# Kernel tuning notes

Hardware: AMD Instinct MI355X
Metric: run time of the kernel (lower is better)

Reference implementation:

```python
import jax, jax.numpy as jnp
import numpy as np

B = 4096
IN_FEATS = 1024
OUT_FEATS = 1024
NUM_HEADS = 16
NUM_MEMS = 4096
HEAD_DIM = OUT_FEATS // NUM_HEADS
TEMPERATURE = 1.0
EPS = 0.0  # original code uses plain jnp.linalg.norm (no eps)


def setup_inputs() -> dict:
    key = jax.random.key(0)
    k1, k2, k3 = jax.random.split(key, 3)
    x = jax.random.normal(k1, (B, IN_FEATS), dtype=jnp.float32)
    # eqx.nn.Linear stores weight as [out, in]; uniform-like init replaced with normal scaled
    W_q = jax.random.normal(k2, (OUT_FEATS, IN_FEATS), dtype=jnp.float32) * (1.0 / np.sqrt(IN_FEATS))
    memories = jax.random.normal(k3, (NUM_HEADS, NUM_MEMS, HEAD_DIM), dtype=jnp.float32) * 0.02
    return {"x": x, "W_q": W_q, "memories": memories}


def reference(x, W_q, memories):
    # q = query_proj(x): [B, out_feats] -> [B, H, d]
    q = (x @ W_q.T).reshape(B, NUM_HEADS, HEAD_DIM)
    # L2-normalize queries and memories along feature dim
    q_norm = q / jnp.linalg.norm(q, axis=-1, keepdims=True)
    mem_norm = memories / jnp.linalg.norm(memories, axis=-1, keepdims=True)
    # cosine-similarity scores: [B, H, M]
    attn_scores = jnp.einsum('bhd,hmd->bhm', q_norm, mem_norm)
    # soft readout (hard=False branch)
    mem_probs = jax.nn.softmax(attn_scores / TEMPERATURE, axis=-1)
    # weighted combine of normalized memories, scaled by sqrt(head_dim)
    out = jnp.einsum('bhm,hmd->bhd', mem_probs, mem_norm) * jnp.sqrt(HEAD_DIM).astype(x.dtype)
    return out.reshape(B, OUT_FEATS)
```

## Files before the change

kernel.cpp:

```cpp
#include <hip/hip_runtime.h>
#include <stdint.h>

#define B_SZ  4096
#define HEADS 16
#define HD    64
#define M_SZ  4096
#define K_IN  1024
#define SW    72
#define LOG2E 1.44269504088896f

typedef _Float16 f16;
typedef f16  f16x2 __attribute__((ext_vector_type(2)));
typedef f16  f16x4 __attribute__((ext_vector_type(4)));
typedef f16  f16x8 __attribute__((ext_vector_type(8)));
typedef float f32x4 __attribute__((ext_vector_type(4)));

union U8 { uint4 u4; f16x8 h8; unsigned short us[8]; };
union U4 { uint2 u2; f16x4 h4; unsigned int ui[2]; unsigned short us[4]; };

__device__ __forceinline__ unsigned short f2h(float f) {
    _Float16 h = (_Float16)f;
    return __builtin_bit_cast(unsigned short, h);
}
__device__ __forceinline__ f16x8 ldsv8(const unsigned short* p) {
    U8 u; u.u4 = *reinterpret_cast<const uint4*>(p); return u.h8;
}

#if __has_builtin(__builtin_amdgcn_exp2f)
#define EXP2F(x) __builtin_amdgcn_exp2f(x)
#else
#define EXP2F(x) __expf((x) * 0.6931471805599453f)
#endif

__device__ __forceinline__ f16x4 pack4(float a, float b, float c, float d) {
#if __has_builtin(__builtin_amdgcn_cvt_pkrtz)
    U4 u;
    u.ui[0] = __builtin_bit_cast(unsigned int, __builtin_amdgcn_cvt_pkrtz(a, b));
    u.ui[1] = __builtin_bit_cast(unsigned int, __builtin_amdgcn_cvt_pkrtz(c, d));
    return u.h4;
#else
    f16x4 r; r[0] = (f16)a; r[1] = (f16)b; r[2] = (f16)c; r[3] = (f16)d;
    return r;
#endif
}

__global__ __launch_bounds__(256) void k_conv(const float* __restrict__ x,
                                              const float* __restrict__ Wq,
                                              unsigned short* __restrict__ xh,
                                              unsigned short* __restrict__ Wh) {
    const int b = blockIdx.x;
    const float* src;
    unsigned short* dst;
    size_t base;
    if (b < 2048) { src = x;  dst = xh; base = (size_t)b * 2048; }
    else          { src = Wq; dst = Wh; base = (size_t)(b - 2048) * 2048; }
    const size_t i = base + (size_t)threadIdx.x * 8;
    float4 f0 = reinterpret_cast<const float4*>(src + i)[0];
    float4 f1 = reinterpret_cast<const float4*>(src + i)[1];
    U8 u;
    u.us[0] = f2h(f0.x); u.us[1] = f2h(f0.y); u.us[2] = f2h(f0.z); u.us[3] = f2h(f0.w);
    u.us[4] = f2h(f1.x); u.us[5] = f2h(f1.y); u.us[6] = f2h(f1.z); u.us[7] = f2h(f1.w);
    *reinterpret_cast<uint4*>(dst + i) = u.u4;
}

__global__ __launch_bounds__(256) void k_prep_mem(const float* __restrict__ mem,
                                                  unsigned short* __restrict__ Af,
                                                  unsigned short* __restrict__ Bf) {
    __shared__ float part[64][4];
    __shared__ float scale[64];
    __shared__ unsigned short Tn[64 * SW];

    const int h  = blockIdx.y;
    const int tl = blockIdx.x;
    const int m0 = tl * 64;
    const int tid = threadIdx.x;
    const int r = tid >> 2;
    const int c = tid & 3;

    const float* src = mem + ((size_t)(h * M_SZ + m0 + r)) * HD + c * 16;
    float v[16];
    float ss = 0.f;
#pragma unroll
    for (int i = 0; i < 4; i++) {
        float4 f = reinterpret_cast<const float4*>(src)[i];
        v[4*i+0] = f.x; v[4*i+1] = f.y; v[4*i+2] = f.z; v[4*i+3] = f.w;
        ss += f.x*f.x + f.y*f.y + f.z*f.z + f.w*f.w;
    }
    part[r][c] = ss;
    __syncthreads();
    if (tid < 64) {
        float s = part[tid][0] + part[tid][1] + part[tid][2] + part[tid][3];
        scale[tid] = rsqrtf(s);
    }
    __syncthreads();
    const float sc = scale[r];

    U8 a, b;
#pragma unroll
    for (int i = 0; i < 8; i++) { a.us[i] = f2h(v[i] * sc); b.us[i] = f2h(v[8 + i] * sc); }
    *reinterpret_cast<uint4*>(&Tn[r * SW + c * 16])     = a.u4;
    *reinterpret_cast<uint4*>(&Tn[r * SW + c * 16 + 8]) = b.u4;
    __syncthreads();

    const int w = tid >> 6, lane = tid & 63;
    const int l15 = lane & 15, quad = lane >> 4;

#pragma unroll
    for (int i = 0; i < 2; i++) {
        const int gs = w * 2 + i, g = gs >> 1, s = gs & 1;
        uint4 vv = *reinterpret_cast<const uint4*>(&Tn[(g * 16 + l15) * SW + s * 32 + quad * 8]);
        unsigned short* dst = Af + (((size_t)(h * 64 + tl) * 8 + gs) * 64 + lane) * 8;
        *reinterpret_cast<uint4*>(dst) = vv;
    }
#pragma unroll
    for (int i = 0; i < 2; i++) {
        const int gnp = w * 2 + i, g = gnp >> 1, np = gnp & 1;
        U8 u;
#pragma unroll
        for (int j = 0; j < 4; j++) {
            u.us[j]     = Tn[(g * 16 + quad * 4 + j) * SW + (2 * np) * 16 + l15];
            u.us[4 + j] = Tn[(g * 16 + quad * 4 + j) * SW + (2 * np + 1) * 16 + l15];
        }
        unsigned short* dst = Bf + (((size_t)(h * 64 + tl) * 8 + gnp) * 64 + lane) * 8;
        *reinterpret_cast<uint4*>(dst) = u.u4;
    }
}

__global__ __launch_bounds__(256) void k_qproj(const unsigned short* __restrict__ xh,
                                               const unsigned short* __restrict__ Wh,
                                               unsigned short* __restrict__ qn) {
    __shared__ unsigned short sbuf[2 * 128 * SW];
    unsigned short* As = sbuf;
    unsigned short* Bs = sbuf + 128 * SW;

    const int b0 = blockIdx.x * 128;
    const int n0 = blockIdx.y * 128;
    const int t = threadIdx.x;
    const int w = t >> 6, lane = t & 63;
    const int wr = w >> 1, wc = w & 1;
    const int l15 = lane & 15, quad = lane >> 4;

    f32x4 acc[4][4] = {};

    const int sr = t >> 1, sh = (t & 1) * 32;
    for (int kb = 0; kb < K_IN; kb += 64) {
        __syncthreads();
        {
            const unsigned short* px = xh + (size_t)(b0 + sr) * K_IN + kb + sh;
            const unsigned short* pw = Wh + (size_t)(n0 + sr) * K_IN + kb + sh;
            uint4 av[4], bv[4];
#pragma unroll
            for (int i = 0; i < 4; i++) av[i] = reinterpret_cast<const uint4*>(px)[i];
#pragma unroll
            for (int i = 0; i < 4; i++) bv[i] = reinterpret_cast<const uint4*>(pw)[i];
#pragma unroll
            for (int i = 0; i < 4; i++) {
                *reinterpret_cast<uint4*>(&As[sr * SW + sh + i * 8]) = av[i];
                *reinterpret_cast<uint4*>(&Bs[sr * SW + sh + i * 8]) = bv[i];
            }
        }
        __syncthreads();

#pragma unroll
        for (int s = 0; s < 2; s++) {
            f16x8 af[4];
#pragma unroll
            for (int qg = 0; qg < 4; qg++)
                af[qg] = ldsv8(&As[(wr * 64 + qg * 16 + l15) * SW + s * 32 + quad * 8]);
#pragma unroll
            for (int g = 0; g < 4; g++) {
                f16x8 bf_ = ldsv8(&Bs[(wc * 64 + g * 16 + l15) * SW + s * 32 + quad * 8]);
#pragma unroll
                for (int qg = 0; qg < 4; qg++)
                    acc[qg][g] = __builtin_amdgcn_mfma_f32_16x16x32_f16(af[qg], bf_, acc[qg][g], 0, 0, 0);
            }
        }
    }

    __syncthreads();
    unsigned short* Ct = sbuf;
#pragma unroll
    for (int qg = 0; qg < 4; qg++) {
        float ssq[4];
#pragma unroll
        for (int r = 0; r < 4; r++) {
            float s = 0.f;
#pragma unroll
            for (int g = 0; g < 4; g++) s += acc[qg][g][r] * acc[qg][g][r];
            ssq[r] = s;
        }
#pragma unroll
        for (int mask = 1; mask <= 8; mask <<= 1)
#pragma unroll
            for (int r = 0; r < 4; r++) ssq[r] += __shfl_xor(ssq[r], mask, 64);
#pragma unroll
        for (int r = 0; r < 4; r++) {
            float inv = rsqrtf(ssq[r]) * LOG2E;
#pragma unroll
            for (int g = 0; g < 4; g++)
                Ct[(wr * 64 + qg * 16 + quad * 4 + r) * 136 + wc * 64 + g * 16 + l15] =
                    f2h(acc[qg][g][r] * inv);
        }
    }
    __syncthreads();

    const int row = t >> 1, half = (t & 1) * 64;
    unsigned short* dq = qn + (size_t)(b0 + row) * 1024 + n0 + half;
#pragma unroll
    for (int i = 0; i < 8; i++)
        reinterpret_cast<uint4*>(dq)[i] = *reinterpret_cast<const uint4*>(&Ct[row * 136 + half + i * 8]);
}

__global__ __launch_bounds__(256, 2) void k_attn(const unsigned short* __restrict__ qn,
                                                 const unsigned short* __restrict__ Af,
                                                 const unsigned short* __restrict__ Bf,
                                                 float* __restrict__ out) {
    const int b = blockIdx.x;
    const int h  = 2 * (b & 7) + (b >> 8);
    const int b0 = ((b >> 3) & 31) * 128;
    const int t = threadIdx.x;
    const int w = t >> 6, lane = t & 63;
    const int l15 = lane & 15, quad = lane >> 4;

    f16x8 qf[2][2];
#pragma unroll
    for (int qg = 0; qg < 2; qg++)
#pragma unroll
        for (int s = 0; s < 2; s++) {
            U8 u;
            u.u4 = *reinterpret_cast<const uint4*>(
                qn + (size_t)(b0 + w * 32 + qg * 16 + l15) * 1024 + h * 64 + s * 32 + quad * 8);
            qf[qg][s] = u.h8;
        }

    const unsigned short* pA = Af + (size_t)h * 64 * 4096 + lane * 8;
    const unsigned short* pB = Bf + (size_t)h * 64 * 4096 + lane * 8;

    f32x4 accO[2][4] = {};
    float lsum[2] = {0.f, 0.f};

    for (int tl = 0; tl < 64; ++tl) {
        const unsigned short* pAt = pA + (size_t)tl * 4096;
        const unsigned short* pBt = pB + (size_t)tl * 4096;

        f16x8 am[8], bw[8];
#pragma unroll
        for (int gs = 0; gs < 8; gs++) {
            U8 u; u.u4 = *reinterpret_cast<const uint4*>(pAt + gs * 512);
            am[gs] = u.h8;
        }
#pragma unroll
        for (int gnp = 0; gnp < 8; gnp++) {
            U8 u; u.u4 = *reinterpret_cast<const uint4*>(pBt + gnp * 512);
            bw[gnp] = u.h8;
        }

        f16x4 pa[2][4];
#pragma unroll
        for (int qg = 0; qg < 2; qg++) {
#pragma unroll
            for (int g = 0; g < 4; g++) {
                f32x4 sc = {0.f, 0.f, 0.f, 0.f};
                sc = __builtin_amdgcn_mfma_f32_16x16x32_f16(am[g * 2 + 0], qf[qg][0], sc, 0, 0, 0);
                sc = __builtin_amdgcn_mfma_f32_16x16x32_f16(am[g * 2 + 1], qf[qg][1], sc, 0, 0, 0);
                float p0 = EXP2F(sc[0]), p1 = EXP2F(sc[1]);
                float p2 = EXP2F(sc[2]), p3 = EXP2F(sc[3]);
                lsum[qg] += (p0 + p1) + (p2 + p3);
                pa[qg][g] = pack4(p0, p1, p2, p3);
            }
        }

#pragma unroll
        for (int g = 0; g < 4; g++) {
#pragma unroll
            for (int np = 0; np < 2; np++) {
                f16x4 blo = __builtin_shufflevector(bw[g * 2 + np], bw[g * 2 + np], 0, 1, 2, 3);
                f16x4 bhi = __builtin_shufflevector(bw[g * 2 + np], bw[g * 2 + np], 4, 5, 6, 7);
#pragma unroll
                for (int qg = 0; qg < 2; qg++) {
                    accO[qg][2 * np]     = __builtin_amdgcn_mfma_f32_16x16x16f16(pa[qg][g], blo, accO[qg][2 * np], 0, 0, 0);
                    accO[qg][2 * np + 1] = __builtin_amdgcn_mfma_f32_16x16x16f16(pa[qg][g], bhi, accO[qg][2 * np + 1], 0, 0, 0);
                }
            }
        }
    }

#pragma unroll
    for (int qg = 0; qg < 2; qg++) {
        float s = lsum[qg];
        s += __shfl_xor(s, 16, 64);
        s += __shfl_xor(s, 32, 64);
        float inv = 8.0f / s;
#pragma unroll
        for (int r = 0; r < 4; r++) {
            float iv = __shfl(inv, quad * 4 + r, 64);
            float* po = out + (size_t)(b0 + w * 32 + qg * 16 + quad * 4 + r) * 1024 + h * 64;
#pragma unroll
            for (int n = 0; n < 4; n++)
                po[n * 16 + l15] = accO[qg][n][r] * iv;
        }
    }
}

extern "C" void kernel_launch(void* const* d_in, const int* in_sizes, int n_in,
                              void* d_out, int out_size, void* d_ws, size_t ws_size,
                              hipStream_t stream) {
    (void)in_sizes; (void)n_in; (void)out_size; (void)ws_size;
    const float* x   = (const float*)d_in[0];
    const float* Wq  = (const float*)d_in[1];
    const float* mem = (const float*)d_in[2];
    float* out = (float*)d_out;

    unsigned short* qn = (unsigned short*)d_ws;
    unsigned short* Af = qn + (size_t)B_SZ * 1024;
    unsigned short* Bf = Af + (size_t)HEADS * 64 * 4096;
    unsigned short* xh = Bf + (size_t)HEADS * 64 * 4096;
    unsigned short* Wh = xh + (size_t)B_SZ * K_IN;

    k_conv    <<<2560, 256, 0, stream>>>(x, Wq, xh, Wh);
    k_prep_mem<<<dim3(64, 16), 256, 0, stream>>>(mem, Af, Bf);
    k_qproj   <<<dim3(32, 8), 256, 0, stream>>>(xh, Wh, qn);
    k_attn    <<<512, 256, 0, stream>>>(qn, Af, Bf, out);
}
```

Measured before the change: 199.0 us.

## Stage memory tiles via async LDS double-buffering and use 16x16x32 MFMA for PV

The attention kernel now loads each memory tile from global straight into a double-buffered LDS array with global_load_lds, prefetching the next tile while the current one is computed. Previously every wave loaded the same tile from global memory on its own. The memory-prep kernel packs both score and value fragments into one interleaved layout whose row order is permuted, so the probability fragments from the score MFMA feed the 16x16x32 MFMA directly. This halves the MFMA count for the PV product. The q-projection tile shrinks to 128x64 with a grid of 512 blocks for better occupancy. The cost is an extra __syncthreads per tile and 32KB of LDS per block, and the correctness of the permuted row mapping rests on careful index arithmetic.

New measurement: 179.1 us. 1.11x faster.

```diff
diff --git a/kernel.cpp b/kernel.cpp
--- a/kernel.cpp
+++ b/kernel.cpp
@@ -10,13 +10,11 @@
 #define LOG2E 1.44269504088896f
 
 typedef _Float16 f16;
-typedef f16  f16x2 __attribute__((ext_vector_type(2)));
 typedef f16  f16x4 __attribute__((ext_vector_type(4)));
 typedef f16  f16x8 __attribute__((ext_vector_type(8)));
 typedef float f32x4 __attribute__((ext_vector_type(4)));
 
-union U8 { uint4 u4; f16x8 h8; unsigned short us[8]; };
-union U4 { uint2 u2; f16x4 h4; unsigned int ui[2]; unsigned short us[4]; };
+union U8 { uint4 u4; f16x8 h8; unsigned int ui[4]; unsigned short us[8]; };
 
 __device__ __forceinline__ unsigned short f2h(float f) {
     _Float16 h = (_Float16)f;
@@ -32,16 +30,10 @@
 #define EXP2F(x) __expf((x) * 0.6931471805599453f)
 #endif
 
-__device__ __forceinline__ f16x4 pack4(float a, float b, float c, float d) {
-#if __has_builtin(__builtin_amdgcn_cvt_pkrtz)
-    U4 u;
-    u.ui[0] = __builtin_bit_cast(unsigned int, __builtin_amdgcn_cvt_pkrtz(a, b));
-    u.ui[1] = __builtin_bit_cast(unsigned int, __builtin_amdgcn_cvt_pkrtz(c, d));
-    return u.h4;
-#else
-    f16x4 r; r[0] = (f16)a; r[1] = (f16)b; r[2] = (f16)c; r[3] = (f16)d;
-    return r;
-#endif
+__device__ __forceinline__ void gload_lds16(const void* g, void* l) {
+    __builtin_amdgcn_global_load_lds(
+        (const __attribute__((address_space(1))) void*)g,
+        (__attribute__((address_space(3))) void*)l, 16, 0, 0);
 }
 
 __global__ __launch_bounds__(256) void k_conv(const float* __restrict__ x,
@@ -64,8 +56,7 @@
 }
 
 __global__ __launch_bounds__(256) void k_prep_mem(const float* __restrict__ mem,
-                                                  unsigned short* __restrict__ Af,
-                                                  unsigned short* __restrict__ Bf) {
+                                                  unsigned short* __restrict__ F) {
     __shared__ float part[64][4];
     __shared__ float scale[64];
     __shared__ unsigned short Tn[64 * SW];
@@ -104,83 +95,80 @@
 
     const int w = tid >> 6, lane = tid & 63;
     const int l15 = lane & 15, quad = lane >> 4;
+    unsigned short* Fd = F + ((size_t)(h * 64 + tl) * 16) * 512;
 
 #pragma unroll
     for (int i = 0; i < 2; i++) {
-        const int gs = w * 2 + i, g = gs >> 1, s = gs & 1;
-        uint4 vv = *reinterpret_cast<const uint4*>(&Tn[(g * 16 + l15) * SW + s * 32 + quad * 8]);
-        unsigned short* dst = Af + (((size_t)(h * 64 + tl) * 8 + gs) * 64 + lane) * 8;
-        *reinterpret_cast<uint4*>(dst) = vv;
+        const int ch = w * 2 + i, g = ch >> 1, s = ch & 1;
+        const int mp = 32 * (g >> 1) + ((l15 >> 2) * 8) + 4 * (g & 1) + (l15 & 3);
+        uint4 vv = *reinterpret_cast<const uint4*>(&Tn[mp * SW + s * 32 + quad * 8]);
+        *reinterpret_cast<uint4*>(Fd + ch * 512 + lane * 8) = vv;
     }
 #pragma unroll
     for (int i = 0; i < 2; i++) {
-        const int gnp = w * 2 + i, g = gnp >> 1, np = gnp & 1;
+        const int c2 = w * 2 + i, p = c2 >> 2, n = c2 & 3;
         U8 u;
 #pragma unroll
-        for (int j = 0; j < 4; j++) {
-            u.us[j]     = Tn[(g * 16 + quad * 4 + j) * SW + (2 * np) * 16 + l15];
-            u.us[4 + j] = Tn[(g * 16 + quad * 4 + j) * SW + (2 * np + 1) * 16 + l15];
-        }
-        unsigned short* dst = Bf + (((size_t)(h * 64 + tl) * 8 + gnp) * 64 + lane) * 8;
-        *reinterpret_cast<uint4*>(dst) = u.u4;
-    }
-}
-
-__global__ __launch_bounds__(256) void k_qproj(const unsigned short* __restrict__ xh,
-                                               const unsigned short* __restrict__ Wh,
-                                               unsigned short* __restrict__ qn) {
-    __shared__ unsigned short sbuf[2 * 128 * SW];
-    unsigned short* As = sbuf;
-    unsigned short* Bs = sbuf + 128 * SW;
+        for (int j = 0; j < 8; j++)
+            u.us[j] = Tn[(32 * p + quad * 8 + j) * SW + n * 16 + l15];
+        *reinterpret_cast<uint4*>(Fd + (8 + c2) * 512 + lane * 8) = u.u4;
+    }
+}
+
+__global__ __launch_bounds__(256, 2) void k_qproj(const unsigned short* __restrict__ xh,
+                                                  const unsigned short* __restrict__ Wh,
+                                                  unsigned short* __restrict__ qn) {
+    __shared__ unsigned short As[128 * SW];
+    __shared__ unsigned short Bs[64 * SW];
 
     const int b0 = blockIdx.x * 128;
-    const int n0 = blockIdx.y * 128;
+    const int n0 = blockIdx.y * 64;
     const int t = threadIdx.x;
     const int w = t >> 6, lane = t & 63;
-    const int wr = w >> 1, wc = w & 1;
     const int l15 = lane & 15, quad = lane >> 4;
 
-    f32x4 acc[4][4] = {};
-
-    const int sr = t >> 1, sh = (t & 1) * 32;
+    f32x4 acc[2][4] = {};
+
     for (int kb = 0; kb < K_IN; kb += 64) {
         __syncthreads();
         {
-            const unsigned short* px = xh + (size_t)(b0 + sr) * K_IN + kb + sh;
-            const unsigned short* pw = Wh + (size_t)(n0 + sr) * K_IN + kb + sh;
-            uint4 av[4], bv[4];
+            const unsigned short* px = xh + (size_t)(b0 + (t >> 1)) * K_IN + kb + (t & 1) * 32;
+            const unsigned short* pw = Wh + (size_t)(n0 + (t >> 2)) * K_IN + kb + (t & 3) * 16;
+            uint4 av[4];
 #pragma unroll
             for (int i = 0; i < 4; i++) av[i] = reinterpret_cast<const uint4*>(px)[i];
-#pragma unroll
-            for (int i = 0; i < 4; i++) bv[i] = reinterpret_cast<const uint4*>(pw)[i];
-#pragma unroll
-            for (int i = 0; i < 4; i++) {
-                *reinterpret_cast<uint4*>(&As[sr * SW + sh + i * 8]) = av[i];
-                *reinterpret_cast<uint4*>(&Bs[sr * SW + sh + i * 8]) = bv[i];
-            }
+            uint4 bv[2];
+#pragma unroll
+            for (int i = 0; i < 2; i++) bv[i] = reinterpret_cast<const uint4*>(pw)[i];
+#pragma unroll
+            for (int i = 0; i < 4; i++)
+                *reinterpret_cast<uint4*>(&As[(t >> 1) * SW + (t & 1) * 32 + i * 8]) = av[i];
+#pragma unroll
+            for (int i = 0; i < 2; i++)
+                *reinterpret_cast<uint4*>(&Bs[(t >> 2) * SW + (t & 3) * 16 + i * 8]) = bv[i];
         }
         __syncthreads();
 
 #pragma unroll
         for (int s = 0; s < 2; s++) {
-            f16x8 af[4];
-#pragma unroll
-            for (int qg = 0; qg < 4; qg++)
-                af[qg] = ldsv8(&As[(wr * 64 + qg * 16 + l15) * SW + s * 32 + quad * 8]);
+            f16x8 af[2];
+#pragma unroll
+            for (int qg = 0; qg < 2; qg++)
+                af[qg] = ldsv8(&As[(w * 32 + qg * 16 + l15) * SW + s * 32 + quad * 8]);
 #pragma unroll
             for (int g = 0; g < 4; g++) {
-                f16x8 bf_ = ldsv8(&Bs[(wc * 64 + g * 16 + l15) * SW + s * 32 + quad * 8]);
-#pragma unroll
-                for (int qg = 0; qg < 4; qg++)
+                f16x8 bf_ = ldsv8(&Bs[(g * 16 + l15) * SW + s * 32 + quad * 8]);
+#pragma unroll
+                for (int qg = 0; qg < 2; qg++)
                     acc[qg][g] = __builtin_amdgcn_mfma_f32_16x16x32_f16(af[qg], bf_, acc[qg][g], 0, 0, 0);
             }
         }
     }
 
     __syncthreads();
-    unsigned short* Ct = sbuf;
-#pragma unroll
-    for (int qg = 0; qg < 4; qg++) {
+    unsigned short* Ct = As;
+#pragma unroll
+    for (int qg = 0; qg < 2; qg++) {
         float ssq[4];
 #pragma unroll
         for (int r = 0; r < 4; r++) {
@@ -198,23 +186,23 @@
             float inv = rsqrtf(ssq[r]) * LOG2E;
 #pragma unroll
             for (int g = 0; g < 4; g++)
-                Ct[(wr * 64 + qg * 16 + quad * 4 + r) * 136 + wc * 64 + g * 16 + l15] =
-                    f2h(acc[qg][g][r] * inv);
-        }
-    }
-    __syncthreads();
-
-    const int row = t >> 1, half = (t & 1) * 64;
+                Ct[(w * 32 + qg * 16 + quad * 4 + r) * SW + g * 16 + l15] = f2h(acc[qg][g][r] * inv);
+        }
+    }
+    __syncthreads();
+
+    const int row = t >> 1, half = (t & 1) * 32;
     unsigned short* dq = qn + (size_t)(b0 + row) * 1024 + n0 + half;
 #pragma unroll
-    for (int i = 0; i < 8; i++)
-        reinterpret_cast<uint4*>(dq)[i] = *reinterpret_cast<const uint4*>(&Ct[row * 136 + half + i * 8]);
+    for (int i = 0; i < 4; i++)
+        reinterpret_cast<uint4*>(dq)[i] = *reinterpret_cast<const uint4*>(&Ct[row * SW + half + i * 8]);
 }
 
 __global__ __launch_bounds__(256, 2) void k_attn(const unsigned short* __restrict__ qn,
-                                                 const unsigned short* __restrict__ Af,
-                                                 const unsigned short* __restrict__ Bf,
+                                                 const unsigned short* __restrict__ F,
                                                  float* __restrict__ out) {
+    __shared__ unsigned short buf[2][8192];
+
     const int b = blockIdx.x;
     const int h  = 2 * (b & 7) + (b >> 8);
     const int b0 = ((b >> 3) & 31) * 128;
@@ -233,54 +221,64 @@
             qf[qg][s] = u.h8;
         }
 
-    const unsigned short* pA = Af + (size_t)h * 64 * 4096 + lane * 8;
-    const unsigned short* pB = Bf + (size_t)h * 64 * 4096 + lane * 8;
+    const unsigned short* Fh = F + (size_t)h * 64 * 8192;
+
+#pragma unroll
+    for (int i = 0; i < 4; i++) {
+        const int ch = w * 4 + i;
+        gload_lds16(Fh + ch * 512 + lane * 8, &buf[0][ch * 512]);
+    }
 
     f32x4 accO[2][4] = {};
     float lsum[2] = {0.f, 0.f};
 
     for (int tl = 0; tl < 64; ++tl) {
-        const unsigned short* pAt = pA + (size_t)tl * 4096;
-        const unsigned short* pBt = pB + (size_t)tl * 4096;
-
+        __syncthreads();
+        const int cur = tl & 1;
+
+        if (tl + 1 < 64) {
+            const unsigned short* gn = Fh + (size_t)(tl + 1) * 8192;
+#pragma unroll
+            for (int i = 0; i < 4; i++) {
+                const int ch = w * 4 + i;
+                gload_lds16(gn + ch * 512 + lane * 8, &buf[cur ^ 1][ch * 512]);
+            }
+        }
+
+        const unsigned short* lb = buf[cur];
         f16x8 am[8], bw[8];
 #pragma unroll
-        for (int gs = 0; gs < 8; gs++) {
-            U8 u; u.u4 = *reinterpret_cast<const uint4*>(pAt + gs * 512);
-            am[gs] = u.h8;
-        }
-#pragma unroll
-        for (int gnp = 0; gnp < 8; gnp++) {
-            U8 u; u.u4 = *reinterpret_cast<const uint4*>(pBt + gnp * 512);
-            bw[gnp] = u.h8;
-        }
-
-        f16x4 pa[2][4];
+        for (int ch = 0; ch < 8; ch++) am[ch] = ldsv8(&lb[ch * 512 + lane * 8]);
+#pragma unroll
+        for (int ch = 0; ch < 8; ch++) bw[ch] = ldsv8(&lb[(8 + ch) * 512 + lane * 8]);
+
 #pragma unroll
         for (int qg = 0; qg < 2; qg++) {
 #pragma unroll
-            for (int g = 0; g < 4; g++) {
-                f32x4 sc = {0.f, 0.f, 0.f, 0.f};
-                sc = __builtin_amdgcn_mfma_f32_16x16x32_f16(am[g * 2 + 0], qf[qg][0], sc, 0, 0, 0);
-                sc = __builtin_amdgcn_mfma_f32_16x16x32_f16(am[g * 2 + 1], qf[qg][1], sc, 0, 0, 0);
-                float p0 = EXP2F(sc[0]), p1 = EXP2F(sc[1]);
-                float p2 = EXP2F(sc[2]), p3 = EXP2F(sc[3]);
-                lsum[qg] += (p0 + p1) + (p2 + p3);
-                pa[qg][g] = pack4(p0, p1, p2, p3);
-            }
-        }
-
-#pragma unroll
-        for (int g = 0; g < 4; g++) {
-#pragma unroll
-            for (int np = 0; np < 2; np++) {
-                f16x4 blo = __builtin_shufflevector(bw[g * 2 + np], bw[g * 2 + np], 0, 1, 2, 3);
-                f16x4 bhi = __builtin_shufflevector(bw[g * 2 + np], bw[g * 2 + np], 4, 5, 6, 7);
-#pragma unroll
-                for (int qg = 0; qg < 2; qg++) {
-                    accO[qg][2 * np]     = __builtin_amdgcn_mfma_f32_16x16x16f16(pa[qg][g], blo, accO[qg][2 * np], 0, 0, 0);
-                    accO[qg][2 * np + 1] = __builtin_amdgcn_mfma_f32_16x16x16f16(pa[qg][g], bhi, accO[qg][2 * np + 1], 0, 0, 0);
-                }
+            for (int p = 0; p < 2; p++) {
+                f32x4 s0 = {0.f, 0.f, 0.f, 0.f}, s1 = {0.f, 0.f, 0.f, 0.f};
+                s0 = __builtin_amdgcn_mfma_f32_16x16x32_f16(am[4*p+0], qf[qg][0], s0, 0, 0, 0);
+                s0 = __builtin_amdgcn_mfma_f32_16x16x32_f16(am[4*p+1], qf[qg][1], s0, 0, 0, 0);
+                s1 = __builtin_amdgcn_mfma_f32_16x16x32_f16(am[4*p+2], qf[qg][0], s1, 0, 0, 0);
+                s1 = __builtin_amdgcn_mfma_f32_16x16x32_f16(am[4*p+3], qf[qg][1], s1, 0, 0, 0);
+
+                float p0 = EXP2F(s0[0]), p1 = EXP2F(s0[1]), p2 = EXP2F(s0[2]), p3 = EXP2F(s0[3]);
+                float p4 = EXP2F(s1[0]), p5 = EXP2F(s1[1]), p6 = EXP2F(s1[2]), p7 = EXP2F(s1[3]);
+                lsum[qg] += ((p0 + p1) + (p2 + p3)) + ((p4 + p5) + (p6 + p7));
+
+                U8 pu;
+#if __has_builtin(__builtin_amdgcn_cvt_pkrtz)
+                pu.ui[0] = __builtin_bit_cast(unsigned int, __builtin_amdgcn_cvt_pkrtz(p0, p1));
+                pu.ui[1] = __builtin_bit_cast(unsigned int, __builtin_amdgcn_cvt_pkrtz(p2, p3));
+                pu.ui[2] = __builtin_bit_cast(unsigned int, __builtin_amdgcn_cvt_pkrtz(p4, p5));
+                pu.ui[3] = __builtin_bit_cast(unsigned int, __builtin_amdgcn_cvt_pkrtz(p6, p7));
+#else
+                pu.us[0]=f2h(p0); pu.us[1]=f2h(p1); pu.us[2]=f2h(p2); pu.us[3]=f2h(p3);
+                pu.us[4]=f2h(p4); pu.us[5]=f2h(p5); pu.us[6]=f2h(p6); pu.us[7]=f2h(p7);
+#endif
+#pragma unroll
+                for (int n = 0; n < 4; n++)
+                    accO[qg][n] = __builtin_amdgcn_mfma_f32_16x16x32_f16(pu.h8, bw[p * 4 + n], accO[qg][n], 0, 0, 0);
             }
         }
     }
@@ -312,13 +310,12 @@
     float* out = (float*)d_out;
 
     unsigned short* qn = (unsigned short*)d_ws;
-    unsigned short* Af = qn + (size_t)B_SZ * 1024;
-    unsigned short* Bf = Af + (size_t)HEADS * 64 * 4096;
-    unsigned short* xh = Bf + (size_t)HEADS * 64 * 4096;
+    unsigned short* F  = qn + (size_t)B_SZ * 1024;
+    unsigned short* xh = F  + (size_t)HEADS * 64 * 16 * 512;
     unsigned short* Wh = xh + (size_t)B_SZ * K_IN;
 
     k_conv    <<<2560, 256, 0, stream>>>(x, Wq, xh, Wh);
-    k_prep_mem<<<dim3(64, 16), 256, 0, stream>>>(mem, Af, Bf);
-    k_qproj   <<<dim3(32, 8), 256, 0, stream>>>(xh, Wh, qn);
-    k_attn    <<<512, 256, 0, stream>>>(qn, Af, Bf, out);
-}
+    k_prep_mem<<<dim3(64, 16), 256, 0, stream>>>(mem, F);
+    k_qproj   <<<dim3(32, 16), 256, 0, stream>>>(xh, Wh, qn);
+    k_attn    <<<512, 256, 0, stream>>>(qn, F, out);
+}
```
